# Performance work log

Measured on AMD Instinct MI355X. Metric: run time of the kernel, lower is better.

The kernel has to match this reference:

```python
import jax, jax.numpy as jnp
import numpy as np

HID = 512
NHEADS = 8
HEAD_DIM = HID // NHEADS  # 64
L = 2048
B = 4
LQ = 128
SCALE = float(np.sqrt(HEAD_DIM))


def _xavier(k, shape):
    lim = float(np.sqrt(6.0 / (shape[0] + shape[1])))
    return jax.random.uniform(k, shape, jnp.float32, -lim, lim)


def setup_inputs() -> dict:
    key = jax.random.key(0)
    ks = jax.random.split(key, 9)
    query = jax.random.normal(ks[0], (L, B, HID), jnp.float32)
    key_t = jax.random.normal(ks[1], (L, B, HID), jnp.float32)
    value = jax.random.normal(ks[2], (L, B, HID), jnp.float32)
    # 1 = pad, 0 = valid (code adds (1-mask).log() to scores)
    key_padding_mask = jax.random.bernoulli(ks[3], 0.1, (B, L)).astype(jnp.float32)
    question_rel_emb = jax.random.normal(ks[4], (LQ, LQ, B, HID), jnp.float32) * 0.02
    Wq = _xavier(ks[5], (HID, HID))
    Wk = _xavier(ks[6], (HID, HID))
    Wv = _xavier(ks[7], (HID, HID))
    Wo = _xavier(ks[8], (HID, HID))
    return dict(query=query, key_t=key_t, value=value,
                key_padding_mask=key_padding_mask,
                question_rel_emb=question_rel_emb,
                Wq=Wq, Wk=Wk, Wv=Wv, Wo=Wo)


def reference(query, key_t, value, key_padding_mask, question_rel_emb, Wq, Wk, Wv, Wo):
    # head_reshape: [L,B,HID] -> [B*K, L, D] (b outer, k inner, matching torch view)
    def heads(x, W):
        y = x @ W.T                                   # [L,B,HID]
        return jnp.swapaxes(y.reshape(L, B * NHEADS, HEAD_DIM), 0, 1)

    q = heads(query, Wq)    # [BK,L,D]
    k = heads(key_t, Wk)
    v = heads(value, Wv)

    attn = jnp.einsum('nld,nmd->nlm', q, k)            # [BK,L,L]

    # question relative bias: proj_key over [Lq,Lq,B,HID] -> [BK,Lq,Lq,D]
    qr = question_rel_emb @ Wk.T
    qr = qr.reshape(LQ, LQ, B * NHEADS, HEAD_DIM).transpose(2, 0, 1, 3)
    bias = jnp.einsum('nijd,nid->nij', qr, q[:, -LQ:])  # [BK,Lq,Lq]
    attn = attn.at[:, -LQ:, -LQ:].add(bias)

    attn = attn / SCALE

    # padding mask: repeat_interleave over batch, add log(1-mask) per key column
    kpm = jnp.repeat(key_padding_mask, NHEADS, axis=0)  # [BK,L]
    attn = attn + jnp.log1p(-kpm)[:, None, :]

    attn = jax.nn.softmax(attn, axis=-1)
    out = jnp.einsum('nlm,nmd->nld', attn, v)           # [BK,L,D]
    out = jnp.swapaxes(out, 0, 1).reshape(L, B, HID) @ Wo.T
    return (out, attn)
```

## Files before the change

### kernel.cpp

```cpp
#include <hip/hip_runtime.h>
#include <hip/hip_bf16.h>


using short8   = __attribute__((ext_vector_type(8))) short;
using short4v  = __attribute__((ext_vector_type(4))) short;
using ushort4v = __attribute__((ext_vector_type(4))) unsigned short;
using f32x4    = __attribute__((ext_vector_type(4))) float;

#define L_T   2048
#define B_T   4
#define HID_T 512
#define HD_T  64
#define LQ_T  128
#define L0_T  1920

__device__ __forceinline__ float b2f(unsigned short u){
  return __uint_as_float(((unsigned int)u) << 16);
}
__device__ __forceinline__ unsigned short f2b(float f){
  unsigned int u = __float_as_uint(f);
  u += 0x7FFFu + ((u >> 16) & 1u);
  return (unsigned short)(u >> 16);
}
__device__ __forceinline__ f32x4 mfma16(short8 a, short8 b, f32x4 c){
  return __builtin_amdgcn_mfma_f32_16x16x32_bf16(a, b, c, 0, 0, 0);
}
#if __has_builtin(__builtin_amdgcn_mfma_f32_16x16x16bf16_1k)
__device__ __forceinline__ f32x4 mfma16k16(short4v a, short4v b, f32x4 c){
  return __builtin_amdgcn_mfma_f32_16x16x16bf16_1k(a, b, c, 0, 0, 0);
}
#else
__device__ __forceinline__ f32x4 mfma16k16(short4v a, short4v b, f32x4 c){
  f32x4 d;
  asm("v_mfma_f32_16x16x16_bf16 %0, %1, %2, %0"
      : "=v"(d) : "v"(a), "v"(b), "0"(c));
  return d;
}
#endif

__global__ __launch_bounds__(256) void k_splitW(const float* __restrict__ w0,
                                                const float* __restrict__ w1,
                                                const float* __restrict__ w2,
                                                const float* __restrict__ w3,
                                                unsigned short* __restrict__ hi,
                                                unsigned short* __restrict__ lo)
{
  int wid = blockIdx.y;
  const float* src = (wid == 0) ? w0 : (wid == 1) ? w1 : (wid == 2) ? w2 : w3;
  int chunk = blockIdx.x * 256 + threadIdx.x;
  int o = chunk >> 7;
  int hpos = (chunk & 127) * 4;
  f32x4 v = ((const f32x4*)src)[chunk];
  ushort4v h4, l4;
  #pragma unroll
  for (int e = 0; e < 4; e++){
    unsigned short h = f2b(v[e]);
    h4[e] = h;
    l4[e] = f2b(v[e] - b2f(h));
  }
  size_t idx = ((size_t)(wid * 512 + (o >> 4) * 16 + (hpos >> 5))) * 512
             + (((hpos & 31) >> 3) * 16 + (o & 15)) * 8 + (hpos & 7);
  *(ushort4v*)(hi + idx) = h4;
  *(ushort4v*)(lo + idx) = l4;
}

__global__ __launch_bounds__(256) void k_proj3(const float* __restrict__ Xq,
                                               const float* __restrict__ Xk,
                                               const float* __restrict__ Xv,
                                               const unsigned short* __restrict__ WhA,
                                               const unsigned short* __restrict__ WlA,
                                               unsigned short* __restrict__ qhp,
                                               unsigned short* __restrict__ qlp,
                                               unsigned short* __restrict__ khp,
                                               unsigned short* __restrict__ klp,
                                               unsigned short* __restrict__ vpk)
{
  int sel = blockIdx.x >> 10;
  int bx  = blockIdx.x & 1023;
  const float* X = (sel == 0) ? Xq : (sel == 1) ? Xk : Xv;
  const short* WH = (const short*)WhA + (size_t)sel * 262144;
  const short* WL = (const short*)WlA + (size_t)sel * 262144;
  unsigned short* ohi = (sel == 0) ? qhp : khp;
  unsigned short* olo = (sel == 0) ? qlp : klp;

  int wv = threadIdx.x >> 6, lane = threadIdx.x & 63;
  int tid = bx * 4 + wv;
  int mt = tid >> 3, nt = tid & 7;
  int row0 = mt * 16, col0 = nt * 64;
  int lhi = lane >> 4, llo = lane & 15;
  int arow = row0 + llo;
  f32x4 acc[4] = {{0,0,0,0},{0,0,0,0},{0,0,0,0},{0,0,0,0}};
  #pragma unroll 4
  for (int k0 = 0; k0 < 512; k0 += 32){
    const float* ap = X + (size_t)arow * 512 + k0 + lhi * 8;
    f32x4 a01 = *(const f32x4*)ap;
    f32x4 a23 = *(const f32x4*)(ap + 4);
    short8 ah, al;
    #pragma unroll
    for (int e = 0; e < 4; e++){
      unsigned short h0 = f2b(a01[e]);
      ah[e] = (short)h0;  al[e] = (short)f2b(a01[e] - b2f(h0));
      unsigned short h1 = f2b(a23[e]);
      ah[e + 4] = (short)h1;  al[e + 4] = (short)f2b(a23[e] - b2f(h1));
    }
    int kk = k0 >> 5;
    #pragma unroll
    for (int cb = 0; cb < 4; cb++){
      size_t bidx = (size_t)(((col0 >> 4) + cb) * 16 + kk) * 512 + lane * 8;
      short8 bh = *(const short8*)(WH + bidx);
      short8 bl = *(const short8*)(WL + bidx);
      acc[cb] = mfma16(ah, bh, acc[cb]);
      acc[cb] = mfma16(al, bh, acc[cb]);
      acc[cb] = mfma16(ah, bl, acc[cb]);
    }
  }
  #pragma unroll
  for (int cb = 0; cb < 4; cb++){
    #pragma unroll
    for (int r = 0; r < 4; r++){
      int row = row0 + lhi * 4 + r;
      int o   = col0 + cb * 16 + llo;
      int l = row >> 2, bb = row & 3;
      int n = bb * 8 + (o >> 6), d = o & 63;
      float v = acc[cb][r];
      if (sel != 2){
        size_t idx = ((size_t)(n * 128 + (l >> 4)) * 2 + (d >> 5)) * 512
                   + (((d & 31) >> 3) * 16 + (l & 15)) * 8 + (d & 7);
        unsigned short h = f2b(v);
        ohi[idx] = h;
        olo[idx] = f2b(v - b2f(h));
      } else {
        int m = l;
        size_t idx = (((size_t)(n * 128 + (m >> 4)) * 4) + (d >> 4)) * 256
                   + ((m & 15) >> 2) * 64 + (d & 15) * 4 + (m & 3);
        vpk[idx] = f2b(v);
      }
    }
  }
}

__global__ __launch_bounds__(256) void k_tb(const unsigned short* __restrict__ qhp,
                                            const unsigned short* __restrict__ qlp,
                                            const float* __restrict__ Wk,
                                            const float* __restrict__ qrem,
                                            float* __restrict__ bias)
{
  int bb = blockIdx.x & 3, i = blockIdx.x >> 2;
  __shared__ float qv[8][64];
  __shared__ float ts[8][512];
  for (int idx = threadIdx.x; idx < 512; idx += 256){
    int kh = idx >> 6, d = idx & 63;
    int n = bb * 8 + kh;
    int row = L0_T + i;
    size_t qidx = ((size_t)(n * 128 + (row >> 4)) * 2 + (d >> 5)) * 512
                + (((d & 31) >> 3) * 16 + (row & 15)) * 8 + (d & 7);
    qv[kh][d] = b2f(qhp[qidx]) + b2f(qlp[qidx]);
  }
  __syncthreads();
  {
    int kh = threadIdx.x >> 5, h0 = (threadIdx.x & 31) * 16;
    f32x4 a0 = {0,0,0,0}, a1 = {0,0,0,0}, a2 = {0,0,0,0}, a3 = {0,0,0,0};
    for (int d = 0; d < 64; d++){
      float qd = qv[kh][d];
      const float* wr = Wk + (size_t)(kh * 64 + d) * 512 + h0;
      a0 += qd * *(const f32x4*)(wr);
      a1 += qd * *(const f32x4*)(wr + 4);
      a2 += qd * *(const f32x4*)(wr + 8);
      a3 += qd * *(const f32x4*)(wr + 12);
    }
    *(f32x4*)&ts[kh][h0]      = a0;
    *(f32x4*)&ts[kh][h0 + 4]  = a1;
    *(f32x4*)&ts[kh][h0 + 8]  = a2;
    *(f32x4*)&ts[kh][h0 + 12] = a3;
  }
  __syncthreads();
  int wv = threadIdx.x >> 6, lane = threadIdx.x & 63;
  for (int j = wv; j < 128; j += 4){
    const float* qr = qrem + (((size_t)i * LQ_T + j) * B_T + bb) * 512;
    f32x4 v0 = *(const f32x4*)(qr + lane * 4);
    f32x4 v1 = *(const f32x4*)(qr + 256 + lane * 4);
    float pl[8];
    #pragma unroll
    for (int kh = 0; kh < 8; kh++){
      f32x4 t0 = *(const f32x4*)&ts[kh][lane * 4];
      f32x4 t1 = *(const f32x4*)&ts[kh][256 + lane * 4];
      pl[kh] = v0[0]*t0[0] + v0[1]*t0[1] + v0[2]*t0[2] + v0[3]*t0[3]
             + v1[0]*t1[0] + v1[1]*t1[1] + v1[2]*t1[2] + v1[3]*t1[3];
    }
    #pragma unroll
    for (int kh = 0; kh < 8; kh++){
      float s = pl[kh];
      #pragma unroll
      for (int msk = 1; msk < 64; msk <<= 1) s += __shfl_xor(s, msk);
      pl[kh] = s;
    }
    if (lane == 0){
      #pragma unroll
      for (int kh = 0; kh < 8; kh++)
        bias[((size_t)(bb * 8 + kh) * LQ_T + i) * LQ_T + j] = pl[kh];
    }
  }
}

__global__ __launch_bounds__(1024, 4) void k_attn(
    const unsigned short* __restrict__ qhp, const unsigned short* __restrict__ qlp,
    const unsigned short* __restrict__ khp, const unsigned short* __restrict__ klp,
    const float* __restrict__ bias, const float* __restrict__ kpm,
    const unsigned short* __restrict__ vpk,
    float* __restrict__ attnF, float* __restrict__ outbk)
{
  __shared__ __attribute__((aligned(16))) float pf[16 * 1024];
  __shared__ float2 red2[16 * 16];
  const int w = threadIdx.x >> 6, lane = threadIdx.x & 63;
  const int lhi = lane >> 4, llo = lane & 15;

  for (int u = blockIdx.x; u < 4096; u += gridDim.x){
    const int n = u >> 7, rb = u & 127;
    const int row0 = rb * 16, bb = n >> 3;

    const short* QH = (const short*)qhp + ((size_t)(n * 128 + rb) * 2) * 512 + lane * 8;
    const short* QL = (const short*)qlp + ((size_t)(n * 128 + rb) * 2) * 512 + lane * 8;
    short8 qh0 = *(const short8*)(QH);
    short8 qh1 = *(const short8*)(QH + 512);
    short8 ql0 = *(const short8*)(QL);
    short8 ql1 = *(const short8*)(QL + 512);
    const short* KH = (const short*)khp + (size_t)n * 131072 + w * 1024 + lane * 8;
    const short* KL = (const short*)klp + (size_t)n * 131072 + w * 1024 + lane * 8;

    float sv[8][4];
    #pragma unroll
    for (int t = 0; t < 8; t++){
      f32x4 acc = {0.f, 0.f, 0.f, 0.f};
      short8 kh0v = *(const short8*)(KH + t * 16384);
      short8 kh1v = *(const short8*)(KH + t * 16384 + 512);
      short8 kl0v = *(const short8*)(KL + t * 16384);
      short8 kl1v = *(const short8*)(KL + t * 16384 + 512);
      acc = mfma16(kh0v, qh0, acc);
      acc = mfma16(kl0v, qh0, acc);
      acc = mfma16(kh0v, ql0, acc);
      acc = mfma16(kh1v, qh1, acc);
      acc = mfma16(kl1v, qh1, acc);
      acc = mfma16(kh1v, ql1, acc);
      if (t == 7 && rb >= 120 && w >= 8){
        int i  = row0 - L0_T + llo;
        int j0 = (w - 8) * 16 + lhi * 4;
        f32x4 bv = *(const f32x4*)(bias + ((size_t)(n * 128 + i)) * 128 + j0);
        acc += bv;
      }
      f32x4 mkv = *(const f32x4*)(kpm + bb * 2048 + (w + t * 16) * 16 + lhi * 4);
      #pragma unroll
      for (int r = 0; r < 4; r++)
        sv[t][r] = acc[r] * 0.125f + ((mkv[r] != 0.f) ? -__builtin_inff() : 0.f);
    }

    float pm = sv[0][0];
    #pragma unroll
    for (int t = 0; t < 8; t++)
      #pragma unroll
      for (int r = 0; r < 4; r++) pm = fmaxf(pm, sv[t][r]);
    pm = fmaxf(pm, __shfl_xor(pm, 16));
    pm = fmaxf(pm, __shfl_xor(pm, 32));
    float es = 0.f;
    #pragma unroll
    for (int t = 0; t < 8; t++)
      #pragma unroll
      for (int r = 0; r < 4; r++){
        float e = __expf(sv[t][r] - pm);
        sv[t][r] = e;
        es += e;
      }
    es += __shfl_xor(es, 16);
    es += __shfl_xor(es, 32);
    if (lane < 16) red2[w * 16 + llo] = make_float2(pm, es);
    asm volatile("s_waitcnt lgkmcnt(0)\n\ts_barrier" ::: "memory");

    float2 c0 = red2[(lhi * 4 + 0) * 16 + llo];
    float2 c1 = red2[(lhi * 4 + 1) * 16 + llo];
    float2 c2 = red2[(lhi * 4 + 2) * 16 + llo];
    float2 c3 = red2[(lhi * 4 + 3) * 16 + llo];
    float mg = fmaxf(fmaxf(c0.x, c1.x), fmaxf(c2.x, c3.x));
    mg = fmaxf(mg, __shfl_xor(mg, 16));
    mg = fmaxf(mg, __shfl_xor(mg, 32));
    float cg = c0.y * __expf(c0.x - mg) + c1.y * __expf(c1.x - mg)
             + c2.y * __expf(c2.x - mg) + c3.y * __expf(c3.x - mg);
    cg += __shfl_xor(cg, 16);
    cg += __shfl_xor(cg, 32);
    float fac = __expf(pm - mg) / cg;

    float* aRow = attnF + ((size_t)(n * L_T + row0 + llo)) * L_T;
    const short* VP = (const short*)vpk + (size_t)n * 131072 + w * 1024 + lane * 4;
    f32x4 pacc0 = {0,0,0,0}, pacc1 = {0,0,0,0}, pacc2 = {0,0,0,0}, pacc3 = {0,0,0,0};
    #pragma unroll
    for (int t = 0; t < 8; t++){
      f32x4 pv;
      #pragma unroll
      for (int r = 0; r < 4; r++) pv[r] = sv[t][r] * fac;
      __builtin_nontemporal_store(pv, (f32x4*)(aRow + (w + t * 16) * 16 + lhi * 4));
      short4v pb;
      #pragma unroll
      for (int r = 0; r < 4; r++) pb[r] = (short)f2b(pv[r]);
      pacc0 = mfma16k16(*(const short4v*)(VP + t * 16384 +   0), pb, pacc0);
      pacc1 = mfma16k16(*(const short4v*)(VP + t * 16384 + 256), pb, pacc1);
      pacc2 = mfma16k16(*(const short4v*)(VP + t * 16384 + 512), pb, pacc2);
      pacc3 = mfma16k16(*(const short4v*)(VP + t * 16384 + 768), pb, pacc3);
    }

    float* pfw = pf + w * 1024 + llo * 64;
    *(f32x4*)(pfw + (( 0 + lhi * 4 + llo * 4) & 63)) = pacc0;
    *(f32x4*)(pfw + ((16 + lhi * 4 + llo * 4) & 63)) = pacc1;
    *(f32x4*)(pfw + ((32 + lhi * 4 + llo * 4) & 63)) = pacc2;
    *(f32x4*)(pfw + ((48 + lhi * 4 + llo * 4) & 63)) = pacc3;
    asm volatile("s_waitcnt lgkmcnt(0)\n\ts_barrier" ::: "memory");
    {
      int q = w, d = lane;
      int slot = (d + q * 4) & 63;
      float s = 0.f;
      #pragma unroll
      for (int ww = 0; ww < 16; ww++) s += pf[ww * 1024 + q * 64 + slot];
      outbk[((size_t)(n * L_T + row0 + q)) * HD_T + d] = s;
    }
  }
}

__global__ __launch_bounds__(256) void k_final(const float* __restrict__ outbk,
                                               const unsigned short* __restrict__ Wh,
                                               const unsigned short* __restrict__ Wl,
                                               float* __restrict__ y)
{
  int wv = threadIdx.x >> 6, lane = threadIdx.x & 63;
  int tid = blockIdx.x * 4 + wv;
  int mt = tid >> 5, nt = tid & 31;
  int row0 = mt * 16, col0 = nt * 16;
  int lhi = lane >> 4, llo = lane & 15;
  int arow = row0 + llo;
  int l = arow >> 2, bb = arow & 3;
  const short* WHs = (const short*)Wh;
  const short* WLs = (const short*)Wl;
  f32x4 acc = {0.f, 0.f, 0.f, 0.f};
  for (int k0 = 0; k0 < 512; k0 += 32){
    int c = k0 + lhi * 8;
    const float* ap = outbk + ((size_t)(bb * 8 + (c >> 6)) * L_T + l) * HD_T + (c & 63);
    f32x4 a01 = *(const f32x4*)ap;
    f32x4 a23 = *(const f32x4*)(ap + 4);
    short8 ahi, alo;
    #pragma unroll
    for (int e = 0; e < 4; e++){
      unsigned short h0 = f2b(a01[e]);
      ahi[e] = (short)h0;  alo[e] = (short)f2b(a01[e] - b2f(h0));
      unsigned short h1 = f2b(a23[e]);
      ahi[e + 4] = (short)h1;  alo[e + 4] = (short)f2b(a23[e] - b2f(h1));
    }
    size_t bidx = (size_t)(nt * 16 + (k0 >> 5)) * 512 + lane * 8;
    short8 bh = *(const short8*)(WHs + bidx);
    short8 bl = *(const short8*)(WLs + bidx);
    acc = mfma16(ahi, bh, acc);
    acc = mfma16(alo, bh, acc);
    acc = mfma16(ahi, bl, acc);
  }
  #pragma unroll
  for (int r = 0; r < 4; r++)
    y[(size_t)(row0 + lhi * 4 + r) * 512 + col0 + llo] = acc[r];
}

extern "C" void kernel_launch(void* const* d_in, const int* in_sizes, int n_in,
                              void* d_out, int out_size, void* d_ws, size_t ws_size,
                              hipStream_t stream)
{
  const float* query = (const float*)d_in[0];
  const float* key_t = (const float*)d_in[1];
  const float* value = (const float*)d_in[2];
  const float* kpm   = (const float*)d_in[3];
  const float* qrem  = (const float*)d_in[4];
  const float* Wq    = (const float*)d_in[5];
  const float* Wk    = (const float*)d_in[6];
  const float* Wv    = (const float*)d_in[7];
  const float* Wo    = (const float*)d_in[8];

  float* outY  = (float*)d_out;
  float* attnF = outY + (size_t)L_T * B_T * HID_T;

  char* wp = (char*)d_ws;
  const size_t SZ8M = (size_t)32 * 2048 * 64 * 2;
  unsigned short* qhp = (unsigned short*)wp; wp += SZ8M;
  unsigned short* qlp = (unsigned short*)wp; wp += SZ8M;
  unsigned short* khp = (unsigned short*)wp; wp += SZ8M;
  unsigned short* klp = (unsigned short*)wp; wp += SZ8M;
  unsigned short* vpk = (unsigned short*)wp; wp += SZ8M;
  unsigned short* whA = (unsigned short*)wp; wp += (size_t)4 * 512 * 512 * 2;
  unsigned short* wlA = (unsigned short*)wp; wp += (size_t)4 * 512 * 512 * 2;
  float* biasb = (float*)wp; wp += (size_t)32 * 128 * 128 * 4;
  float* outbk = (float*)wp; wp += (size_t)32 * 2048 * 64 * 4;

  const size_t WSTEP = (size_t)512 * 512;

  k_splitW<<<dim3(256, 4), 256, 0, stream>>>(Wq, Wk, Wv, Wo, whA, wlA);
  k_proj3<<<3072, 256, 0, stream>>>(query, key_t, value, whA, wlA,
                                    qhp, qlp, khp, klp, vpk);
  k_tb<<<512, 256, 0, stream>>>(qhp, qlp, Wk, qrem, biasb);
  k_attn<<<512, 1024, 0, stream>>>(qhp, qlp, khp, klp, biasb, kpm,
                                   vpk, attnF, outbk);
  k_final<<<4096, 256, 0, stream>>>(outbk, whA + 3 * WSTEP, wlA + 3 * WSTEP, outY);
}
```

Before: 526.9 us.

## Process two 16-row query blocks per iteration to reuse K and V loads

The attention kernel now handles a pair of adjacent 16-row blocks per loop iteration, so each K and V fragment loaded from global memory feeds MFMAs for both blocks. The grid shrinks from 512 to 256 workgroups, each running a fixed 8 iterations. The aim is to halve K/V load traffic per output row and raise MFMA density. The cost is roughly doubled register pressure for scores and accumulators, an extra barrier pair for the second output reduction, and fewer workgroups to fill the device.

New measurement: 518.0 us. Within noise of the previous version (-1.7%).

```diff
diff --git a/kernel.cpp b/kernel.cpp
--- a/kernel.cpp
+++ b/kernel.cpp
@@ -210,106 +210,170 @@
     float* __restrict__ attnF, float* __restrict__ outbk)
 {
   __shared__ __attribute__((aligned(16))) float pf[16 * 1024];
-  __shared__ float2 red2[16 * 16];
+  __shared__ float2 red2[2 * 256];
   const int w = threadIdx.x >> 6, lane = threadIdx.x & 63;
   const int lhi = lane >> 4, llo = lane & 15;
 
-  for (int u = blockIdx.x; u < 4096; u += gridDim.x){
-    const int n = u >> 7, rb = u & 127;
-    const int row0 = rb * 16, bb = n >> 3;
-
-    const short* QH = (const short*)qhp + ((size_t)(n * 128 + rb) * 2) * 512 + lane * 8;
-    const short* QL = (const short*)qlp + ((size_t)(n * 128 + rb) * 2) * 512 + lane * 8;
-    short8 qh0 = *(const short8*)(QH);
-    short8 qh1 = *(const short8*)(QH + 512);
-    short8 ql0 = *(const short8*)(QL);
-    short8 ql1 = *(const short8*)(QL + 512);
+  for (int j = 0; j < 8; ++j){
+    const int p = blockIdx.x + (j << 8);
+    const int n = p >> 6, rbp = p & 63;
+    const int rbA = rbp * 2, rbB = rbA + 1;
+    const int row0A = rbA * 16, row0B = rbB * 16, bb = n >> 3;
+
+    const short* QHA = (const short*)qhp + ((size_t)(n * 128 + rbA) * 2) * 512 + lane * 8;
+    const short* QLA = (const short*)qlp + ((size_t)(n * 128 + rbA) * 2) * 512 + lane * 8;
+    const short* QHB = (const short*)qhp + ((size_t)(n * 128 + rbB) * 2) * 512 + lane * 8;
+    const short* QLB = (const short*)qlp + ((size_t)(n * 128 + rbB) * 2) * 512 + lane * 8;
+    short8 qhA0 = *(const short8*)(QHA);
+    short8 qhA1 = *(const short8*)(QHA + 512);
+    short8 qlA0 = *(const short8*)(QLA);
+    short8 qlA1 = *(const short8*)(QLA + 512);
+    short8 qhB0 = *(const short8*)(QHB);
+    short8 qhB1 = *(const short8*)(QHB + 512);
+    short8 qlB0 = *(const short8*)(QLB);
+    short8 qlB1 = *(const short8*)(QLB + 512);
     const short* KH = (const short*)khp + (size_t)n * 131072 + w * 1024 + lane * 8;
     const short* KL = (const short*)klp + (size_t)n * 131072 + w * 1024 + lane * 8;
 
-    float sv[8][4];
+    float svA[8][4], svB[8][4];
     #pragma unroll
     for (int t = 0; t < 8; t++){
-      f32x4 acc = {0.f, 0.f, 0.f, 0.f};
       short8 kh0v = *(const short8*)(KH + t * 16384);
       short8 kh1v = *(const short8*)(KH + t * 16384 + 512);
       short8 kl0v = *(const short8*)(KL + t * 16384);
       short8 kl1v = *(const short8*)(KL + t * 16384 + 512);
-      acc = mfma16(kh0v, qh0, acc);
-      acc = mfma16(kl0v, qh0, acc);
-      acc = mfma16(kh0v, ql0, acc);
-      acc = mfma16(kh1v, qh1, acc);
-      acc = mfma16(kl1v, qh1, acc);
-      acc = mfma16(kh1v, ql1, acc);
-      if (t == 7 && rb >= 120 && w >= 8){
-        int i  = row0 - L0_T + llo;
+      f32x4 aA = {0.f, 0.f, 0.f, 0.f};
+      f32x4 aB = {0.f, 0.f, 0.f, 0.f};
+      aA = mfma16(kh0v, qhA0, aA);
+      aA = mfma16(kl0v, qhA0, aA);
+      aA = mfma16(kh0v, qlA0, aA);
+      aA = mfma16(kh1v, qhA1, aA);
+      aA = mfma16(kl1v, qhA1, aA);
+      aA = mfma16(kh1v, qlA1, aA);
+      aB = mfma16(kh0v, qhB0, aB);
+      aB = mfma16(kl0v, qhB0, aB);
+      aB = mfma16(kh0v, qlB0, aB);
+      aB = mfma16(kh1v, qhB1, aB);
+      aB = mfma16(kl1v, qhB1, aB);
+      aB = mfma16(kh1v, qlB1, aB);
+      if (t == 7 && rbp >= 60 && w >= 8){
         int j0 = (w - 8) * 16 + lhi * 4;
-        f32x4 bv = *(const f32x4*)(bias + ((size_t)(n * 128 + i)) * 128 + j0);
-        acc += bv;
+        int iA = row0A - L0_T + llo;
+        int iB = row0B - L0_T + llo;
+        aA += *(const f32x4*)(bias + ((size_t)(n * 128 + iA)) * 128 + j0);
+        aB += *(const f32x4*)(bias + ((size_t)(n * 128 + iB)) * 128 + j0);
       }
       f32x4 mkv = *(const f32x4*)(kpm + bb * 2048 + (w + t * 16) * 16 + lhi * 4);
       #pragma unroll
-      for (int r = 0; r < 4; r++)
-        sv[t][r] = acc[r] * 0.125f + ((mkv[r] != 0.f) ? -__builtin_inff() : 0.f);
-    }
-
-    float pm = sv[0][0];
+      for (int r = 0; r < 4; r++){
+        float mk = (mkv[r] != 0.f) ? -__builtin_inff() : 0.f;
+        svA[t][r] = aA[r] * 0.125f + mk;
+        svB[t][r] = aB[r] * 0.125f + mk;
+      }
+    }
+
+    float pmA = svA[0][0], pmB = svB[0][0];
     #pragma unroll
     for (int t = 0; t < 8; t++)
       #pragma unroll
-      for (int r = 0; r < 4; r++) pm = fmaxf(pm, sv[t][r]);
-    pm = fmaxf(pm, __shfl_xor(pm, 16));
-    pm = fmaxf(pm, __shfl_xor(pm, 32));
-    float es = 0.f;
+      for (int r = 0; r < 4; r++){
+        pmA = fmaxf(pmA, svA[t][r]);
+        pmB = fmaxf(pmB, svB[t][r]);
+      }
+    pmA = fmaxf(pmA, __shfl_xor(pmA, 16));
+    pmA = fmaxf(pmA, __shfl_xor(pmA, 32));
+    pmB = fmaxf(pmB, __shfl_xor(pmB, 16));
+    pmB = fmaxf(pmB, __shfl_xor(pmB, 32));
+    float esA = 0.f, esB = 0.f;
     #pragma unroll
     for (int t = 0; t < 8; t++)
       #pragma unroll
       for (int r = 0; r < 4; r++){
-        float e = __expf(sv[t][r] - pm);
-        sv[t][r] = e;
-        es += e;
-      }
-    es += __shfl_xor(es, 16);
-    es += __shfl_xor(es, 32);
-    if (lane < 16) red2[w * 16 + llo] = make_float2(pm, es);
+        float eA = __expf(svA[t][r] - pmA);
+        float eB = __expf(svB[t][r] - pmB);
+        svA[t][r] = eA;  esA += eA;
+        svB[t][r] = eB;  esB += eB;
+      }
+    esA += __shfl_xor(esA, 16);
+    esA += __shfl_xor(esA, 32);
+    esB += __shfl_xor(esB, 16);
+    esB += __shfl_xor(esB, 32);
+    if (lane < 16){
+      red2[w * 16 + llo]       = make_float2(pmA, esA);
+      red2[256 + w * 16 + llo] = make_float2(pmB, esB);
+    }
     asm volatile("s_waitcnt lgkmcnt(0)\n\ts_barrier" ::: "memory");
 
-    float2 c0 = red2[(lhi * 4 + 0) * 16 + llo];
-    float2 c1 = red2[(lhi * 4 + 1) * 16 + llo];
-    float2 c2 = red2[(lhi * 4 + 2) * 16 + llo];
-    float2 c3 = red2[(lhi * 4 + 3) * 16 + llo];
-    float mg = fmaxf(fmaxf(c0.x, c1.x), fmaxf(c2.x, c3.x));
-    mg = fmaxf(mg, __shfl_xor(mg, 16));
-    mg = fmaxf(mg, __shfl_xor(mg, 32));
-    float cg = c0.y * __expf(c0.x - mg) + c1.y * __expf(c1.x - mg)
-             + c2.y * __expf(c2.x - mg) + c3.y * __expf(c3.x - mg);
-    cg += __shfl_xor(cg, 16);
-    cg += __shfl_xor(cg, 32);
-    float fac = __expf(pm - mg) / cg;
-
-    float* aRow = attnF + ((size_t)(n * L_T + row0 + llo)) * L_T;
+    float facA, facB;
+    {
+      float2 c0 = red2[(lhi * 4 + 0) * 16 + llo];
+      float2 c1 = red2[(lhi * 4 + 1) * 16 + llo];
+      float2 c2 = red2[(lhi * 4 + 2) * 16 + llo];
+      float2 c3 = red2[(lhi * 4 + 3) * 16 + llo];
+      float mg = fmaxf(fmaxf(c0.x, c1.x), fmaxf(c2.x, c3.x));
+      mg = fmaxf(mg, __shfl_xor(mg, 16));
+      mg = fmaxf(mg, __shfl_xor(mg, 32));
+      float cg = c0.y * __expf(c0.x - mg) + c1.y * __expf(c1.x - mg)
+               + c2.y * __expf(c2.x - mg) + c3.y * __expf(c3.x - mg);
+      cg += __shfl_xor(cg, 16);
+      cg += __shfl_xor(cg, 32);
+      facA = __expf(pmA - mg) / cg;
+    }
+    {
+      float2 c0 = red2[256 + (lhi * 4 + 0) * 16 + llo];
+      float2 c1 = red2[256 + (lhi * 4 + 1) * 16 + llo];
+      float2 c2 = red2[256 + (lhi * 4 + 2) * 16 + llo];
+      float2 c3 = red2[256 + (lhi * 4 + 3) * 16 + llo];
+      float mg = fmaxf(fmaxf(c0.x, c1.x), fmaxf(c2.x, c3.x));
+      mg = fmaxf(mg, __shfl_xor(mg, 16));
+      mg = fmaxf(mg, __shfl_xor(mg, 32));
+      float cg = c0.y * __expf(c0.x - mg) + c1.y * __expf(c1.x - mg)
+               + c2.y * __expf(c2.x - mg) + c3.y * __expf(c3.x - mg);
+      cg += __shfl_xor(cg, 16);
+      cg += __shfl_xor(cg, 32);
+      facB = __expf(pmB - mg) / cg;
+    }
+
+    float* aRowA = attnF + ((size_t)(n * L_T + row0A + llo)) * L_T;
+    float* aRowB = attnF + ((size_t)(n * L_T + row0B + llo)) * L_T;
     const short* VP = (const short*)vpk + (size_t)n * 131072 + w * 1024 + lane * 4;
-    f32x4 pacc0 = {0,0,0,0}, pacc1 = {0,0,0,0}, pacc2 = {0,0,0,0}, pacc3 = {0,0,0,0};
+    f32x4 pA0 = {0,0,0,0}, pA1 = {0,0,0,0}, pA2 = {0,0,0,0}, pA3 = {0,0,0,0};
+    f32x4 pB0 = {0,0,0,0}, pB1 = {0,0,0,0}, pB2 = {0,0,0,0}, pB3 = {0,0,0,0};
     #pragma unroll
     for (int t = 0; t < 8; t++){
-      f32x4 pv;
-      #pragma unroll
-      for (int r = 0; r < 4; r++) pv[r] = sv[t][r] * fac;
-      __builtin_nontemporal_store(pv, (f32x4*)(aRow + (w + t * 16) * 16 + lhi * 4));
-      short4v pb;
-      #pragma unroll
-      for (int r = 0; r < 4; r++) pb[r] = (short)f2b(pv[r]);
-      pacc0 = mfma16k16(*(const short4v*)(VP + t * 16384 +   0), pb, pacc0);
-      pacc1 = mfma16k16(*(const short4v*)(VP + t * 16384 + 256), pb, pacc1);
-      pacc2 = mfma16k16(*(const short4v*)(VP + t * 16384 + 512), pb, pacc2);
-      pacc3 = mfma16k16(*(const short4v*)(VP + t * 16384 + 768), pb, pacc3);
+      short4v v0 = *(const short4v*)(VP + t * 16384 +   0);
+      short4v v1 = *(const short4v*)(VP + t * 16384 + 256);
+      short4v v2 = *(const short4v*)(VP + t * 16384 + 512);
+      short4v v3 = *(const short4v*)(VP + t * 16384 + 768);
+      f32x4 pvA, pvB;
+      #pragma unroll
+      for (int r = 0; r < 4; r++){
+        pvA[r] = svA[t][r] * facA;
+        pvB[r] = svB[t][r] * facB;
+      }
+      __builtin_nontemporal_store(pvA, (f32x4*)(aRowA + (w + t * 16) * 16 + lhi * 4));
+      __builtin_nontemporal_store(pvB, (f32x4*)(aRowB + (w + t * 16) * 16 + lhi * 4));
+      short4v pbA, pbB;
+      #pragma unroll
+      for (int r = 0; r < 4; r++){
+        pbA[r] = (short)f2b(pvA[r]);
+        pbB[r] = (short)f2b(pvB[r]);
+      }
+      pA0 = mfma16k16(v0, pbA, pA0);
+      pA1 = mfma16k16(v1, pbA, pA1);
+      pA2 = mfma16k16(v2, pbA, pA2);
+      pA3 = mfma16k16(v3, pbA, pA3);
+      pB0 = mfma16k16(v0, pbB, pB0);
+      pB1 = mfma16k16(v1, pbB, pB1);
+      pB2 = mfma16k16(v2, pbB, pB2);
+      pB3 = mfma16k16(v3, pbB, pB3);
     }
 
     float* pfw = pf + w * 1024 + llo * 64;
-    *(f32x4*)(pfw + (( 0 + lhi * 4 + llo * 4) & 63)) = pacc0;
-    *(f32x4*)(pfw + ((16 + lhi * 4 + llo * 4) & 63)) = pacc1;
-    *(f32x4*)(pfw + ((32 + lhi * 4 + llo * 4) & 63)) = pacc2;
-    *(f32x4*)(pfw + ((48 + lhi * 4 + llo * 4) & 63)) = pacc3;
+    *(f32x4*)(pfw + (( 0 + lhi * 4 + llo * 4) & 63)) = pA0;
+    *(f32x4*)(pfw + ((16 + lhi * 4 + llo * 4) & 63)) = pA1;
+    *(f32x4*)(pfw + ((32 + lhi * 4 + llo * 4) & 63)) = pA2;
+    *(f32x4*)(pfw + ((48 + lhi * 4 + llo * 4) & 63)) = pA3;
     asm volatile("s_waitcnt lgkmcnt(0)\n\ts_barrier" ::: "memory");
     {
       int q = w, d = lane;
@@ -317,7 +381,21 @@
       float s = 0.f;
       #pragma unroll
       for (int ww = 0; ww < 16; ww++) s += pf[ww * 1024 + q * 64 + slot];
-      outbk[((size_t)(n * L_T + row0 + q)) * HD_T + d] = s;
+      outbk[((size_t)(n * L_T + row0A + q)) * HD_T + d] = s;
+    }
+    asm volatile("s_waitcnt lgkmcnt(0)\n\ts_barrier" ::: "memory");
+    *(f32x4*)(pfw + (( 0 + lhi * 4 + llo * 4) & 63)) = pB0;
+    *(f32x4*)(pfw + ((16 + lhi * 4 + llo * 4) & 63)) = pB1;
+    *(f32x4*)(pfw + ((32 + lhi * 4 + llo * 4) & 63)) = pB2;
+    *(f32x4*)(pfw + ((48 + lhi * 4 + llo * 4) & 63)) = pB3;
+    asm volatile("s_waitcnt lgkmcnt(0)\n\ts_barrier" ::: "memory");
+    {
+      int q = w, d = lane;
+      int slot = (d + q * 4) & 63;
+      float s = 0.f;
+      #pragma unroll
+      for (int ww = 0; ww < 16; ww++) s += pf[ww * 1024 + q * 64 + slot];
+      outbk[((size_t)(n * L_T + row0B + q)) * HD_T + d] = s;
     }
   }
 }
@@ -397,7 +475,7 @@
   k_proj3<<<3072, 256, 0, stream>>>(query, key_t, value, whA, wlA,
                                     qhp, qlp, khp, klp, vpk);
   k_tb<<<512, 256, 0, stream>>>(qhp, qlp, Wk, qrem, biasb);
-  k_attn<<<512, 1024, 0, stream>>>(qhp, qlp, khp, klp, biasb, kpm,
+  k_attn<<<256, 1024, 0, stream>>>(qhp, qlp, khp, klp, biasb, kpm,
                                    vpk, attnF, outbk);
   k_final<<<4096, 256, 0, stream>>>(outbk, whA + 3 * WSTEP, wlA + 3 * WSTEP, outY);
 }
```
